# Kernel optimization log

Measured on AMD Instinct MI355X. Metric: run time of the kernel, lower is better.

The kernel has to match this reference:

```python
import jax, jax.numpy as jnp
import numpy as np

D_MODEL = 1024
HEADS = 16
D_K = D_MODEL // HEADS
D_FF = 4096
EPS = 1e-5


def _layernorm(x, gamma, beta):
    mu = jnp.mean(x, axis=-1, keepdims=True)
    var = jnp.var(x, axis=-1, keepdims=True)
    return (x - mu) * jax.lax.rsqrt(var + EPS) * gamma + beta


def setup_inputs() -> dict:
    key = jax.random.key(0)
    ks = jax.random.split(key, 8)
    s = 0.02
    return {
        "x": jax.random.normal(ks[0], (4, 2048, D_MODEL), dtype=jnp.float32),
        "wq": jax.random.normal(ks[1], (D_MODEL, D_MODEL), dtype=jnp.float32) * s,
        "wk": jax.random.normal(ks[2], (D_MODEL, D_MODEL), dtype=jnp.float32) * s,
        "wv": jax.random.normal(ks[3], (D_MODEL, D_MODEL), dtype=jnp.float32) * s,
        "wo": jax.random.normal(ks[4], (D_MODEL, D_MODEL), dtype=jnp.float32) * s,
        "w1": jax.random.normal(ks[5], (D_MODEL, D_FF), dtype=jnp.float32) * s,
        "b1": jnp.zeros((D_FF,), dtype=jnp.float32),
        "w2": jax.random.normal(ks[6], (D_FF, D_MODEL), dtype=jnp.float32) * s,
        "b2": jnp.zeros((D_MODEL,), dtype=jnp.float32),
        "g1": jnp.ones((D_MODEL,), dtype=jnp.float32),
        "be1": jnp.zeros((D_MODEL,), dtype=jnp.float32),
        "g2": jnp.ones((D_MODEL,), dtype=jnp.float32),
        "be2": jnp.zeros((D_MODEL,), dtype=jnp.float32),
    }


def reference(x, wq, wk, wv, wo, w1, b1, w2, b2, g1, be1, g2, be2):
    B, S, D = x.shape
    # --- multi-head self-attention (dropout = identity at eval) ---
    q = (x @ wq).reshape(B, S, HEADS, D_K).transpose(0, 2, 1, 3)  # [B,H,S,dk]
    k = (x @ wk).reshape(B, S, HEADS, D_K).transpose(0, 2, 1, 3)
    v = (x @ wv).reshape(B, S, HEADS, D_K).transpose(0, 2, 1, 3)
    scores = jnp.einsum("bhqd,bhkd->bhqk", q, k) / jnp.sqrt(jnp.float32(D_K))
    attn = jax.nn.softmax(scores, axis=-1)
    ctx = jnp.einsum("bhqk,bhkd->bhqd", attn, v)
    ctx = ctx.transpose(0, 2, 1, 3).reshape(B, S, D)
    attn_out = ctx @ wo
    # --- add & norm 1 ---
    h = _layernorm(x + attn_out, g1, be1)
    # --- FFN ---
    ffn = jax.nn.relu(h @ w1 + b1) @ w2 + b2
    # --- add & norm 2 ---
    return _layernorm(h + ffn, g2, be2)
```

## Files before the change

kernel.cpp:

```cpp
#include <hip/hip_runtime.h>
#include <hip/hip_bf16.h>


typedef float  floatx2  __attribute__((ext_vector_type(2)));
typedef float  floatx4  __attribute__((ext_vector_type(4)));
typedef float  floatx16 __attribute__((ext_vector_type(16)));
typedef short  shortx8  __attribute__((ext_vector_type(8)));
typedef short  shortx4  __attribute__((ext_vector_type(4)));
typedef int    intx4    __attribute__((ext_vector_type(4)));
typedef unsigned uintx2 __attribute__((ext_vector_type(2)));

__device__ __forceinline__ short f2bs(float f) {
    union { float f; unsigned u; } a; a.f = f;
    unsigned r = a.u + 0x7fffu + ((a.u >> 16) & 1u);
    return (short)(r >> 16);
}

__device__ __forceinline__ float fexp2(float x) {
#if __has_builtin(__builtin_amdgcn_exp2f)
    return __builtin_amdgcn_exp2f(x);
#else
    return __expf(0.6931471805599453f * x);
#endif
}

__device__ __forceinline__ void lane32swap(unsigned& a, unsigned& b) {
#if __has_builtin(__builtin_amdgcn_permlane32_swap)
    uintx2 r = __builtin_amdgcn_permlane32_swap(a, b, false, false);
    a = r[0]; b = r[1];
#else
    int hl = (threadIdx.x & 63) >> 5;
    unsigned ta = (unsigned)__shfl_xor((int)a, 32);
    unsigned tb = (unsigned)__shfl_xor((int)b, 32);
    unsigned na = hl ? tb : a;
    unsigned nb = hl ? b : ta;
    a = na; b = nb;
#endif
}

__device__ __forceinline__ void gload16(const short* g, short* l) {
    __builtin_amdgcn_global_load_lds(
        (const __attribute__((address_space(1))) void*)g,
        (__attribute__((address_space(3))) void*)l,
        16, 0, 0);
}

#define WAITV(n) asm volatile("s_waitcnt vmcnt(" #n ")" ::: "memory")
#define FENCE    asm volatile("" ::: "memory")

__device__ __forceinline__ void trans_tile(const float* __restrict__ in,
                                           short* __restrict__ out,
                                           int N, int K, int k0, int n0,
                                           short (*t)[68]) {
    const int tid = threadIdx.x;
    const int r = tid >> 4, c4 = (tid & 15) * 4;
#pragma unroll
    for (int i = 0; i < 4; ++i) {
        int k = r + i * 16;
        floatx4 v = *(const floatx4*)(in + (size_t)(k0 + k) * N + n0 + c4);
        shortx4 s;
#pragma unroll
        for (int j = 0; j < 4; ++j) s[j] = f2bs(v[j]);
        *(shortx4*)(&t[k][c4]) = s;
    }
    __syncthreads();
#pragma unroll
    for (int i = 0; i < 4; ++i) {
        int n = r + i * 16;
        shortx4 s;
#pragma unroll
        for (int j = 0; j < 4; ++j) s[j] = t[c4 + j][n];
        *(shortx4*)(out + (size_t)(n0 + n) * K + k0 + c4) = s;
    }
}

__global__ __launch_bounds__(256) void prep_kernel(
    const float* __restrict__ wq, const float* __restrict__ wk,
    const float* __restrict__ wv, const float* __restrict__ wo,
    const float* __restrict__ w1, const float* __restrict__ w2,
    const float* __restrict__ x,
    short* wqt, short* wkt, short* wvt, short* wot,
    short* w1t, short* w2t, short* xb)
{
    __shared__ __align__(16) short t[64][68];
    const int bid = blockIdx.x;
    if (bid < 1024) {
        const int widx = bid >> 8, local = bid & 255;
        const float* in = widx == 0 ? wq : widx == 1 ? wk : widx == 2 ? wv : wo;
        short* out = widx == 0 ? wqt : widx == 1 ? wkt : widx == 2 ? wvt : wot;
        trans_tile(in, out, 1024, 1024, (local & 15) * 64, (local >> 4) * 64, t);
    } else if (bid < 2048) {
        const int local = bid - 1024;
        trans_tile(w1, w1t, 4096, 1024, (local & 15) * 64, (local >> 4) * 64, t);
    } else if (bid < 3072) {
        const int local = bid - 2048;
        trans_tile(w2, w2t, 1024, 4096, (local & 63) * 64, (local >> 6) * 64, t);
    } else {
        const int local = bid - 3072;
#pragma unroll
        for (int j = 0; j < 4; ++j) {
            int i = local * 1024 + j * 256 + threadIdx.x;
            floatx4 v = *(const floatx4*)(x + (size_t)i * 4);
            shortx4 o;
            o[0] = f2bs(v[0]); o[1] = f2bs(v[1]); o[2] = f2bs(v[2]); o[3] = f2bs(v[3]);
            *(shortx4*)(xb + (size_t)i * 4) = o;
        }
    }
}

template<int EPI, int BN>
__global__ __launch_bounds__(512, 2) void gemm256(
    const short* __restrict__ A, const short* __restrict__ Bt, const int K, const int N,
    short* __restrict__ outb, float* __restrict__ outf,
    const float* __restrict__ bias, const float* __restrict__ resf)
{
    constexpr int BUFSZ = 16384 + BN * 64;
    constexpr int NF = BN / 64;
    constexpr int NBUF = (BN == 128) ? 3 : 2;
    __shared__ __align__(16) short Ls[NBUF * BUFSZ];
    const int tid = threadIdx.x;
    const int w = tid >> 6, lane = tid & 63;
    const int quad = lane >> 4, l16 = lane & 15;
    const int wm = w >> 2, wn = w & 3;
    const int bx = blockIdx.x, by = blockIdx.y;

    const int srow = w * 16 + (lane >> 3);
    const int uc0 = ((lane & 7) ^ ((lane >> 4) & 7)) * 8;
    const int uc1 = ((lane & 7) ^ (((lane >> 4) + 4) & 7)) * 8;
    const short* aS0 = A  + (size_t)(by * 256 + srow) * K + uc0;
    const short* aS1 = A  + (size_t)(by * 256 + srow + 8) * K + uc1;
    const short* bS0 = Bt + (size_t)(bx * BN + srow) * K + uc0;
    const short* bS1 = Bt + (size_t)(bx * BN + srow + 8) * K + uc1;
    const size_t hK = (size_t)128 * K;
    const int wsl = w * 1024;

    const int rswz = (l16 >> 1) & 7;
    const int ru0 = (quad ^ rswz) * 8;
    const int ru1 = ((4 + quad) ^ rswz) * 8;
    const int aRd = (wm * 64 + l16) * 64;
    const int bRd = (wn * 32 + l16) * 64;

    floatx4 acc[8][NF] = {};
    shortx8 af[4][2], blo[2][2], bhi[2][2];

#define S_A0(buf, kc) { short* p = Ls + (buf) * BUFSZ + wsl;         gload16(aS0 + (kc), p);      gload16(aS1 + (kc), p + 512);      FENCE; }
#define S_A1(buf, kc) { short* p = Ls + (buf) * BUFSZ + 8192 + wsl;  gload16(aS0 + hK + (kc), p); gload16(aS1 + hK + (kc), p + 512); FENCE; }
#define S_B0(buf, kc) { short* p = Ls + (buf) * BUFSZ + 16384 + wsl; gload16(bS0 + (kc), p);      gload16(bS1 + (kc), p + 512);      FENCE; }
#define S_B1(buf, kc) { short* p = Ls + (buf) * BUFSZ + 24576 + wsl; gload16(bS0 + hK + (kc), p); gload16(bS1 + hK + (kc), p + 512); FENCE; }
#define MF(a, b, c) c = __builtin_amdgcn_mfma_f32_16x16x32_bf16(a, b, c, 0, 0, 0)

#define RD_ALO(Ab) {                                                      \
_Pragma("unroll")                                                         \
        for (int mf = 0; mf < 4; ++mf) {                                  \
            af[mf][0] = *(const shortx8*)((Ab) + aRd + mf * 1024 + ru0);  \
            af[mf][1] = *(const shortx8*)((Ab) + aRd + mf * 1024 + ru1);  \
        } }
#define RD_AHI(Ab) {                                                      \
_Pragma("unroll")                                                         \
        for (int mf = 0; mf < 4; ++mf) {                                  \
            af[mf][0] = *(const shortx8*)((Ab) + aRd + 8192 + mf * 1024 + ru0); \
            af[mf][1] = *(const shortx8*)((Ab) + aRd + 8192 + mf * 1024 + ru1); \
        } }
#define RD_BLO(Bb) {                                                      \
_Pragma("unroll")                                                         \
        for (int nf = 0; nf < 2; ++nf) {                                  \
            blo[nf][0] = *(const shortx8*)((Bb) + bRd + nf * 1024 + ru0); \
            blo[nf][1] = *(const shortx8*)((Bb) + bRd + nf * 1024 + ru1); \
        } }
#define MFMA_LO { __builtin_amdgcn_s_setprio(1);                          \
_Pragma("unroll")                                                         \
        for (int mf = 0; mf < 4; ++mf)                                    \
_Pragma("unroll")                                                         \
            for (int nf = 0; nf < 2; ++nf) {                              \
                MF(af[mf][0], blo[nf][0], acc[mf][nf]);                   \
                MF(af[mf][1], blo[nf][1], acc[mf][nf]);                   \
            }                                                             \
        __builtin_amdgcn_s_setprio(0); }
#define MFMA_HI { __builtin_amdgcn_s_setprio(1);                          \
_Pragma("unroll")                                                         \
        for (int mf = 0; mf < 4; ++mf)                                    \
_Pragma("unroll")                                                         \
            for (int nf = 0; nf < 2; ++nf) {                              \
                MF(af[mf][0], blo[nf][0], acc[4 + mf][nf]);               \
                MF(af[mf][1], blo[nf][1], acc[4 + mf][nf]);               \
            }                                                             \
        __builtin_amdgcn_s_setprio(0); }

    const int NT = K >> 6;

    if constexpr (BN == 256) {
        S_A0(0, 0) S_B0(0, 0) S_B1(0, 0) S_A1(0, 0)
        for (int t = 0; t < NT - 1; ++t) {
            const int rb = t & 1, wbuf = rb ^ 1, kc = (t + 1) * 64;
            const short* Ab = Ls + rb * BUFSZ;
            const short* Bb = Ab + 16384;
            WAITV(4); __builtin_amdgcn_s_barrier(); FENCE;
            RD_ALO(Ab) RD_BLO(Bb)
            S_A0(wbuf, kc)
            MFMA_LO
            WAITV(4); __builtin_amdgcn_s_barrier(); FENCE;
#pragma unroll
            for (int nf = 0; nf < 2; ++nf) {
                bhi[nf][0] = *(const shortx8*)(Bb + bRd + 8192 + nf * 1024 + ru0);
                bhi[nf][1] = *(const shortx8*)(Bb + bRd + 8192 + nf * 1024 + ru1);
            }
            S_B0(wbuf, kc)
            __builtin_amdgcn_s_setprio(1);
#pragma unroll
            for (int mf = 0; mf < 4; ++mf)
#pragma unroll
                for (int nf = 0; nf < 2; ++nf) {
                    MF(af[mf][0], bhi[nf][0], acc[mf][2 + nf]);
                    MF(af[mf][1], bhi[nf][1], acc[mf][2 + nf]);
                }
            __builtin_amdgcn_s_setprio(0);
            WAITV(4); __builtin_amdgcn_s_barrier(); FENCE;
            RD_AHI(Ab)
            S_B1(wbuf, kc)
            MFMA_HI
            S_A1(wbuf, kc)
            __builtin_amdgcn_s_setprio(1);
#pragma unroll
            for (int mf = 0; mf < 4; ++mf)
#pragma unroll
                for (int nf = 0; nf < 2; ++nf) {
                    MF(af[mf][0], bhi[nf][0], acc[4 + mf][2 + nf]);
                    MF(af[mf][1], bhi[nf][1], acc[4 + mf][2 + nf]);
                }
            __builtin_amdgcn_s_setprio(0);
        }
        {
            const int rb = (NT - 1) & 1;
            const short* Ab = Ls + rb * BUFSZ;
            const short* Bb = Ab + 16384;
            WAITV(4); __builtin_amdgcn_s_barrier(); FENCE;
            RD_ALO(Ab) RD_BLO(Bb)
            MFMA_LO
            WAITV(2); __builtin_amdgcn_s_barrier(); FENCE;
#pragma unroll
            for (int nf = 0; nf < 2; ++nf) {
                bhi[nf][0] = *(const shortx8*)(Bb + bRd + 8192 + nf * 1024 + ru0);
                bhi[nf][1] = *(const shortx8*)(Bb + bRd + 8192 + nf * 1024 + ru1);
            }
            __builtin_amdgcn_s_setprio(1);
#pragma unroll
            for (int mf = 0; mf < 4; ++mf)
#pragma unroll
                for (int nf = 0; nf < 2; ++nf) {
                    MF(af[mf][0], bhi[nf][0], acc[mf][2 + nf]);
                    MF(af[mf][1], bhi[nf][1], acc[mf][2 + nf]);
                }
            __builtin_amdgcn_s_setprio(0);
            WAITV(0); __builtin_amdgcn_s_barrier(); FENCE;
            RD_AHI(Ab)
            __builtin_amdgcn_s_setprio(1);
#pragma unroll
            for (int mf = 0; mf < 4; ++mf)
#pragma unroll
                for (int nf = 0; nf < 2; ++nf) {
                    MF(af[mf][0], blo[nf][0], acc[4 + mf][nf]);
                    MF(af[mf][1], blo[nf][1], acc[4 + mf][nf]);
                    MF(af[mf][0], bhi[nf][0], acc[4 + mf][2 + nf]);
                    MF(af[mf][1], bhi[nf][1], acc[4 + mf][2 + nf]);
                }
            __builtin_amdgcn_s_setprio(0);
        }
    } else {
        S_A0(0, 0) S_B0(0, 0) S_A1(0, 0)
        S_A0(1, 64) S_B0(1, 64) S_A1(1, 64)
        for (int t = 0; t < NT - 2; ++t) {
            const int rb = t % 3, pb = (t + 2) % 3, kc = (t + 2) * 64;
            const short* Ab = Ls + rb * BUFSZ;
            const short* Bb = Ab + 16384;
            WAITV(8); __builtin_amdgcn_s_barrier(); FENCE;
            RD_ALO(Ab) RD_BLO(Bb)
            S_A0(pb, kc)
            MFMA_LO
            WAITV(8); __builtin_amdgcn_s_barrier(); FENCE;
            RD_AHI(Ab)
            S_B0(pb, kc) S_A1(pb, kc)
            MFMA_HI
        }
        {
            const int rb = (NT - 2) % 3;
            const short* Ab = Ls + rb * BUFSZ;
            const short* Bb = Ab + 16384;
            WAITV(8); __builtin_amdgcn_s_barrier(); FENCE;
            RD_ALO(Ab) RD_BLO(Bb)
            MFMA_LO
            WAITV(6); __builtin_amdgcn_s_barrier(); FENCE;
            RD_AHI(Ab)
            MFMA_HI
        }
        {
            const int rb = (NT - 1) % 3;
            const short* Ab = Ls + rb * BUFSZ;
            const short* Bb = Ab + 16384;
            WAITV(2); __builtin_amdgcn_s_barrier(); FENCE;
            RD_ALO(Ab) RD_BLO(Bb)
            MFMA_LO
            WAITV(0); __builtin_amdgcn_s_barrier(); FENCE;
            RD_AHI(Ab)
            MFMA_HI
        }
    }

#pragma unroll
    for (int mf = 0; mf < 8; ++mf) {
        const int grow0 = by * 256 + (mf >> 2) * 128 + wm * 64 + (mf & 3) * 16 + quad * 4;
#pragma unroll
        for (int nf = 0; nf < NF; ++nf) {
            int gcol;
            if constexpr (BN == 256)
                gcol = bx * 256 + (nf >> 1) * 128 + wn * 32 + (nf & 1) * 16 + l16;
            else
                gcol = bx * 128 + wn * 32 + nf * 16 + l16;
            const floatx4 a = acc[mf][nf];
            if constexpr (EPI == 5) {
                const int slice = gcol >> 10, c = gcol & 1023;
                const int hh = c >> 6, d = c & 63;
                const int b = grow0 >> 11, s0 = grow0 & 2047;
                if (slice == 2) {
                    short* vt = outb + ((size_t)16 << 20);
                    shortx4 pkv;
#pragma unroll
                    for (int r = 0; r < 4; ++r) pkv[r] = f2bs(a[r]);
                    *(shortx4*)(vt + ((size_t)((b * 16 + hh) * 64 + d)) * 2048 + s0) = pkv;
                } else {
                    short* dst = slice ? (outb + ((size_t)8 << 20)) : outb;
                    float sc = slice ? 1.f : 0.125f * 1.4426950408889634f;
#pragma unroll
                    for (int r = 0; r < 4; ++r)
                        dst[(((size_t)(b * 16 + hh)) * 2048 + (s0 + r)) * 64 + d] =
                            f2bs(a[r] * sc);
                }
            } else if constexpr (EPI == 1) {
                const float bv = bias[gcol];
#pragma unroll
                for (int r = 0; r < 4; ++r) {
                    float v = fmaxf(a[r] + bv, 0.f);
                    outb[(size_t)(grow0 + r) * N + gcol] = f2bs(v);
                }
            } else if constexpr (EPI == 2) {
#pragma unroll
                for (int r = 0; r < 4; ++r)
                    outf[(size_t)(grow0 + r) * N + gcol] =
                        a[r] + resf[(size_t)(grow0 + r) * N + gcol];
            } else if constexpr (EPI == 3) {
                const float bv = bias[gcol];
#pragma unroll
                for (int r = 0; r < 4; ++r)
                    outf[(size_t)(grow0 + r) * N + gcol] =
                        a[r] + bv + resf[(size_t)(grow0 + r) * N + gcol];
            }
        }
    }
#undef S_A0
#undef S_A1
#undef S_B0
#undef S_B1
#undef MF
#undef RD_ALO
#undef RD_AHI
#undef RD_BLO
#undef MFMA_LO
#undef MFMA_HI
}

__global__ __launch_bounds__(256) void ln_kernel(
    const float* __restrict__ in, float* __restrict__ outf, short* __restrict__ outb,
    const float* __restrict__ g, const float* __restrict__ be, int writeB)
{
    __shared__ float red[8];
    const int row = blockIdx.x, tid = threadIdx.x;
    const float* p = in + (size_t)row * 1024;
    floatx4 v = *(const floatx4*)(p + tid * 4);
    float s = v[0] + v[1] + v[2] + v[3];
    float q = v[0] * v[0] + v[1] * v[1] + v[2] * v[2] + v[3] * v[3];
#pragma unroll
    for (int off = 32; off; off >>= 1) {
        s += __shfl_xor(s, off);
        q += __shfl_xor(q, off);
    }
    int w = tid >> 6, lane = tid & 63;
    if (lane == 0) { red[w] = s; red[4 + w] = q; }
    __syncthreads();
    s = red[0] + red[1] + red[2] + red[3];
    q = red[4] + red[5] + red[6] + red[7];
    float mean = s * (1.f / 1024.f);
    float var = q * (1.f / 1024.f) - mean * mean;
    float rs = rsqrtf(var + 1e-5f);
    floatx4 gv = *(const floatx4*)(g + tid * 4);
    floatx4 bv = *(const floatx4*)(be + tid * 4);
    floatx4 o4;
#pragma unroll
    for (int i = 0; i < 4; ++i) o4[i] = (v[i] - mean) * rs * gv[i] + bv[i];
    *(floatx4*)(outf + (size_t)row * 1024 + tid * 4) = o4;
    if (writeB) {
        shortx4 ob;
#pragma unroll
        for (int i = 0; i < 4; ++i) ob[i] = f2bs(o4[i]);
        *(shortx4*)(outb + (size_t)row * 1024 + tid * 4) = ob;
    }
}

__global__ __launch_bounds__(256, 4) void attn_kernel(
    const short* __restrict__ Q, const short* __restrict__ K,
    const short* __restrict__ Vt, short* __restrict__ ctx)
{
    __shared__ __align__(16) short Ls[16384];
    short* Ks = Ls;
    short* Vs = Ls + 8192;
    const int tid = threadIdx.x;
    const int q0 = blockIdx.x * 128, bh = blockIdx.y;
    const int w = tid >> 6, lane = tid & 63, l31 = lane & 31, hl = lane >> 5;
    const size_t sb = (size_t)bh * 2048 * 64;

    shortx8 qf[4];
#pragma unroll
    for (int ks = 0; ks < 4; ++ks)
        qf[ks] = *(const shortx8*)(Q + sb + (size_t)(q0 + w * 32 + l31) * 64 + ks * 16 + hl * 8);

    const short* kSrc = K + sb + (size_t)(w * 32 + (lane >> 3)) * 64
                        + (((lane & 7) ^ ((lane >> 3) & 7)) * 8);
    int vOff[4];
#pragma unroll
    for (int j = 0; j < 4; ++j)
        vOff[j] = (w * 16 + j * 4 + (lane >> 4)) * 2048
                  + (((lane & 15) ^ (j * 4 + (lane >> 4))) * 8);
    const short* vBase = Vt + sb;

    const int kx = l31 & 7, vx = l31 & 15;

    floatx16 o[2] = {};
    floatx2 rsA = {0.f, 0.f}, rsB = {0.f, 0.f};
    const floatx16 z = {};

#define LD_AK(mt, ks) (*(const shortx8*)(Ks + ((mt) * 32 + l31) * 64 + ((((ks) * 2 + hl) ^ kx)) * 8))
#define LD_AV(mtd, mt, ksl) (*(const shortx8*)(Vs + ((mtd) * 32 + l31) * 128 + ((((mt) * 4 + (ksl) * 2 + hl) ^ vx)) * 8))

    for (int kt = 0; kt < 16; ++kt) {
        const int kv0 = kt * 128;
        __syncthreads();
#pragma unroll
        for (int j = 0; j < 4; ++j)
            gload16(kSrc + (size_t)kv0 * 64 + j * 512, Ks + (w * 4 + j) * 512);
#pragma unroll
        for (int j = 0; j < 4; ++j)
            gload16(vBase + vOff[j] + kv0, Vs + (w * 4 + j) * 512);
        WAITV(0);
        __syncthreads();

#pragma unroll
        for (int mt = 0; mt < 4; ++mt) {
            floatx16 sc;
            __builtin_amdgcn_s_setprio(1);
            sc = __builtin_amdgcn_mfma_f32_32x32x16_bf16(LD_AK(mt, 0), qf[0], z, 0, 0, 0);
            sc = __builtin_amdgcn_mfma_f32_32x32x16_bf16(LD_AK(mt, 1), qf[1], sc, 0, 0, 0);
            sc = __builtin_amdgcn_mfma_f32_32x32x16_bf16(LD_AK(mt, 2), qf[2], sc, 0, 0, 0);
            sc = __builtin_amdgcn_mfma_f32_32x32x16_bf16(LD_AK(mt, 3), qf[3], sc, 0, 0, 0);
            __builtin_amdgcn_s_setprio(0);
            floatx2 ps2[8];
#pragma unroll
            for (int i = 0; i < 8; ++i) {
                ps2[i][0] = fexp2(sc[2 * i]);
                ps2[i][1] = fexp2(sc[2 * i + 1]);
            }
#pragma unroll
            for (int i = 0; i < 8; i += 2) { rsA += ps2[i]; rsB += ps2[i + 1]; }
            unsigned pk[8];
#pragma unroll
            for (int i = 0; i < 8; ++i) {
                union { __hip_bfloat162 h; unsigned u; } cv;
                cv.h = __float22bfloat162_rn(make_float2(ps2[i][0], ps2[i][1]));
                pk[i] = cv.u;
            }
            lane32swap(pk[0], pk[2]);
            lane32swap(pk[1], pk[3]);
            lane32swap(pk[4], pk[6]);
            lane32swap(pk[5], pk[7]);
            __builtin_amdgcn_s_setprio(1);
#pragma unroll
            for (int ksl = 0; ksl < 2; ++ksl) {
                union { unsigned i[4]; shortx8 s8; } fr;
                fr.i[0] = pk[4 * ksl];     fr.i[1] = pk[4 * ksl + 1];
                fr.i[2] = pk[4 * ksl + 2]; fr.i[3] = pk[4 * ksl + 3];
#pragma unroll
                for (int mtd = 0; mtd < 2; ++mtd)
                    o[mtd] = __builtin_amdgcn_mfma_f32_32x32x16_bf16(LD_AV(mtd, mt, ksl), fr.s8, o[mtd], 0, 0, 0);
            }
            __builtin_amdgcn_s_setprio(0);
        }
    }
#undef LD_AK
#undef LD_AV

    float rsum = rsA[0] + rsA[1] + rsB[0] + rsB[1];
    float tot = rsum + __shfl_xor(rsum, 32);
    float inv = 1.f / tot;

    __syncthreads();
    short* O_lds = Ls;
#pragma unroll
    for (int mtd = 0; mtd < 2; ++mtd)
#pragma unroll
        for (int g = 0; g < 4; ++g) {
            shortx4 p4;
#pragma unroll
            for (int r = 0; r < 4; ++r) p4[r] = f2bs(o[mtd][4 * g + r] * inv);
            *(shortx4*)(O_lds + (w * 32 + l31) * 72 + mtd * 32 + g * 8 + hl * 4) = p4;
        }
    __syncthreads();
    const int b = bh >> 4, head = bh & 15;
#pragma unroll
    for (int it = 0; it < 4; ++it) {
        int idx = it * 256 + tid;
        int q = idx >> 3, ch = idx & 7;
        shortx8 v = *(const shortx8*)(O_lds + q * 72 + ch * 8);
        *(shortx8*)(ctx + ((size_t)(b * 2048 + q0 + q)) * 1024 + head * 64 + ch * 8) = v;
    }
}

extern "C" void kernel_launch(void* const* d_in, const int* in_sizes, int n_in,
                              void* d_out, int out_size, void* d_ws, size_t ws_size,
                              hipStream_t stream) {
    const float* x   = (const float*)d_in[0];
    const float* wq  = (const float*)d_in[1];
    const float* wk  = (const float*)d_in[2];
    const float* wv  = (const float*)d_in[3];
    const float* wo  = (const float*)d_in[4];
    const float* w1  = (const float*)d_in[5];
    const float* b1  = (const float*)d_in[6];
    const float* w2  = (const float*)d_in[7];
    const float* b2  = (const float*)d_in[8];
    const float* g1p = (const float*)d_in[9];
    const float* be1 = (const float*)d_in[10];
    const float* g2p = (const float*)d_in[11];
    const float* be2 = (const float*)d_in[12];
    float* out = (float*)d_out;

    char* ws = (char*)d_ws;
    const size_t MB = 1ull << 20;
    short* wqt  = (short*)(ws + 0 * MB);
    short* wkt  = (short*)(ws + 2 * MB);
    short* wvt  = (short*)(ws + 4 * MB);
    short* wot  = (short*)(ws + 6 * MB);
    short* w1t  = (short*)(ws + 8 * MB);
    short* w2t  = (short*)(ws + 16 * MB);
    short* xb   = (short*)(ws + 24 * MB);
    short* Qb   = (short*)(ws + 40 * MB);
    short* Kb   = (short*)(ws + 56 * MB);
    short* Vtg  = (short*)(ws + 72 * MB);
    short* ctxb = (short*)(ws + 88 * MB);
    float* tf   = (float*)(ws + 104 * MB);
    short* hb   = (short*)(ws + 136 * MB);
    short* f1b  = (short*)(ws + 40 * MB);

    prep_kernel<<<5120, 256, 0, stream>>>(wq, wk, wv, wo, w1, w2, x,
                                          wqt, wkt, wvt, wot, w1t, w2t, xb);

    gemm256<5, 128><<<dim3(24, 32), 512, 0, stream>>>(xb, wqt, 1024, 3072, Qb, nullptr, nullptr, nullptr);
    attn_kernel<<<dim3(16, 64), 256, 0, stream>>>(Qb, Kb, Vtg, ctxb);
    gemm256<2, 128><<<dim3(8, 32), 512, 0, stream>>>(ctxb, wot, 1024, 1024, nullptr, tf, nullptr, x);
    ln_kernel<<<8192, 256, 0, stream>>>(tf, tf, hb, g1p, be1, 1);
    gemm256<1, 256><<<dim3(16, 32), 512, 0, stream>>>(hb, w1t, 1024, 4096, f1b, nullptr, b1, nullptr);
    gemm256<3, 128><<<dim3(8, 32), 512, 0, stream>>>(f1b, w2t, 4096, 1024, nullptr, out, b2, tf);
    ln_kernel<<<8192, 256, 0, stream>>>(out, out, nullptr, g2p, be2, 0);
}
```

Measured before the change: 382.9 us.

## Double-buffer K/V tiles in attention kernel with smaller 64-key stages

Restructures the attention loop to process 64-key tiles with two LDS buffers, issuing the next tile's async global-to-LDS loads before computing on the current one. It also drops one of the two barriers per iteration. The goal is to overlap K/V memory traffic with the MFMA and exp work instead of stalling on each load. In exchange there are twice as many iterations, each with less compute per barrier, and the V layout and swizzle are changed to 64-wide rows.

```diff
diff --git a/kernel.cpp b/kernel.cpp
--- a/kernel.cpp
+++ b/kernel.cpp
@@ -409,8 +409,6 @@
     const short* __restrict__ Vt, short* __restrict__ ctx)
 {
     __shared__ __align__(16) short Ls[16384];
-    short* Ks = Ls;
-    short* Vs = Ls + 8192;
     const int tid = threadIdx.x;
     const int q0 = blockIdx.x * 128, bh = blockIdx.y;
     const int w = tid >> 6, lane = tid & 63, l31 = lane & 31, hl = lane >> 5;
@@ -421,44 +419,46 @@
     for (int ks = 0; ks < 4; ++ks)
         qf[ks] = *(const shortx8*)(Q + sb + (size_t)(q0 + w * 32 + l31) * 64 + ks * 16 + hl * 8);
 
-    const short* kSrc = K + sb + (size_t)(w * 32 + (lane >> 3)) * 64
-                        + (((lane & 7) ^ ((lane >> 3) & 7)) * 8);
-    int vOff[4];
-#pragma unroll
-    for (int j = 0; j < 4; ++j)
-        vOff[j] = (w * 16 + j * 4 + (lane >> 4)) * 2048
-                  + (((lane & 15) ^ (j * 4 + (lane >> 4))) * 8);
-    const short* vBase = Vt + sb;
-
-    const int kx = l31 & 7, vx = l31 & 15;
+    const int srow = w * 8 + (lane >> 3);
+    const int sunit = ((lane & 7) ^ (lane >> 3)) * 8;
+    const short* kSrc = K + sb + (size_t)srow * 64 + sunit;
+    const short* vSrc = Vt + sb + (size_t)srow * 2048 + sunit;
+    const int sdst = w * 512;
+
+    const int kx = l31 & 7;
 
     floatx16 o[2] = {};
     floatx2 rsA = {0.f, 0.f}, rsB = {0.f, 0.f};
     const floatx16 z = {};
 
-#define LD_AK(mt, ks) (*(const shortx8*)(Ks + ((mt) * 32 + l31) * 64 + ((((ks) * 2 + hl) ^ kx)) * 8))
-#define LD_AV(mtd, mt, ksl) (*(const shortx8*)(Vs + ((mtd) * 32 + l31) * 128 + ((((mt) * 4 + (ksl) * 2 + hl) ^ vx)) * 8))
-
-    for (int kt = 0; kt < 16; ++kt) {
-        const int kv0 = kt * 128;
-        __syncthreads();
-#pragma unroll
-        for (int j = 0; j < 4; ++j)
-            gload16(kSrc + (size_t)kv0 * 64 + j * 512, Ks + (w * 4 + j) * 512);
-#pragma unroll
-        for (int j = 0; j < 4; ++j)
-            gload16(vBase + vOff[j] + kv0, Vs + (w * 4 + j) * 512);
+#define STAGE(buf, kv0) { \
+    short* kb = Ls + (buf) * 8192 + sdst; \
+    gload16(kSrc + (size_t)(kv0) * 64, kb); \
+    gload16(kSrc + (size_t)(kv0) * 64 + 2048, kb + 2048); \
+    gload16(vSrc + (kv0), kb + 4096); \
+    gload16(vSrc + (kv0) + 65536, kb + 6144); \
+    FENCE; }
+
+#define LD_AK(B, mt, ks) (*(const shortx8*)((B) + ((mt) * 32 + l31) * 64 + ((((ks) * 2 + hl) ^ kx)) * 8))
+#define LD_AV(B, mtd, mt, ksl) (*(const shortx8*)((B) + 4096 + ((mtd) * 32 + l31) * 64 + ((((mt) * 4 + (ksl) * 2 + hl) ^ kx)) * 8))
+
+    STAGE(0, 0)
+
+    for (int kt = 0; kt < 32; ++kt) {
         WAITV(0);
-        __syncthreads();
-
-#pragma unroll
-        for (int mt = 0; mt < 4; ++mt) {
+        __builtin_amdgcn_s_barrier();
+        FENCE;
+        if (kt < 31) STAGE((kt + 1) & 1, (kt + 1) * 64)
+        const short* B = Ls + (kt & 1) * 8192;
+
+#pragma unroll
+        for (int mt = 0; mt < 2; ++mt) {
             floatx16 sc;
             __builtin_amdgcn_s_setprio(1);
-            sc = __builtin_amdgcn_mfma_f32_32x32x16_bf16(LD_AK(mt, 0), qf[0], z, 0, 0, 0);
-            sc = __builtin_amdgcn_mfma_f32_32x32x16_bf16(LD_AK(mt, 1), qf[1], sc, 0, 0, 0);
-            sc = __builtin_amdgcn_mfma_f32_32x32x16_bf16(LD_AK(mt, 2), qf[2], sc, 0, 0, 0);
-            sc = __builtin_amdgcn_mfma_f32_32x32x16_bf16(LD_AK(mt, 3), qf[3], sc, 0, 0, 0);
+            sc = __builtin_amdgcn_mfma_f32_32x32x16_bf16(LD_AK(B, mt, 0), qf[0], z, 0, 0, 0);
+            sc = __builtin_amdgcn_mfma_f32_32x32x16_bf16(LD_AK(B, mt, 1), qf[1], sc, 0, 0, 0);
+            sc = __builtin_amdgcn_mfma_f32_32x32x16_bf16(LD_AK(B, mt, 2), qf[2], sc, 0, 0, 0);
+            sc = __builtin_amdgcn_mfma_f32_32x32x16_bf16(LD_AK(B, mt, 3), qf[3], sc, 0, 0, 0);
             __builtin_amdgcn_s_setprio(0);
             floatx2 ps2[8];
 #pragma unroll
@@ -487,11 +487,12 @@
                 fr.i[2] = pk[4 * ksl + 2]; fr.i[3] = pk[4 * ksl + 3];
 #pragma unroll
                 for (int mtd = 0; mtd < 2; ++mtd)
-                    o[mtd] = __builtin_amdgcn_mfma_f32_32x32x16_bf16(LD_AV(mtd, mt, ksl), fr.s8, o[mtd], 0, 0, 0);
+                    o[mtd] = __builtin_amdgcn_mfma_f32_32x32x16_bf16(LD_AV(B, mtd, mt, ksl), fr.s8, o[mtd], 0, 0, 0);
             }
             __builtin_amdgcn_s_setprio(0);
         }
     }
+#undef STAGE
 #undef LD_AK
 #undef LD_AV
 
```

Measured after the change: 384.1 us. Within noise of the previous version (+0.3%).
